# Kernel optimization log

Measured on AMD Instinct MI355X. Metric: run time of the kernel, lower is better.

## Reference

```python
import jax, jax.numpy as jnp
import numpy as np

B, T, D, H = 4, 2048, 1024, 16


def setup_inputs() -> dict:
    key = jax.random.key(0)
    ks = jax.random.split(key, 5)
    s = 0.02  # keep activations sane
    return {
        "x": jax.random.normal(ks[0], (B, T, D), jnp.float32),
        "Wq": jax.random.normal(ks[1], (D, D), jnp.float32) * s,
        "bq": jnp.zeros((D,), jnp.float32),
        "Wk": jax.random.normal(ks[2], (D, D), jnp.float32) * s,
        "bk": jnp.zeros((D,), jnp.float32),
        "Wv": jax.random.normal(ks[3], (D, D), jnp.float32) * s,
        "bv": jnp.zeros((D,), jnp.float32),
        "Wo": jax.random.normal(ks[4], (D, D), jnp.float32) * s,
        "bo": jnp.zeros((D,), jnp.float32),
    }


def _split_heads(t):  # (B,T,D) -> (B,H,T,d)
    b, s, d = t.shape
    return t.reshape(b, s, H, d // H).transpose(0, 2, 1, 3)


def reference(x, Wq, bq, Wk, bk, Wv, bv, Wo, bo):
    d_k = D // H
    q = _split_heads(x @ Wq + bq)  # (B,H,T,d)
    k = _split_heads(x @ Wk + bk)
    v = _split_heads(x @ Wv + bv)
    # scaled dot-product similarities (B,H,T,T)
    scores = jnp.einsum("bhqd,bhkd->bhqk", q, k) / jnp.sqrt(jnp.asarray(d_k, x.dtype))
    # causal mask: masked_fill(tril==0, -inf)
    causal = jnp.tril(jnp.ones((T, T), bool))
    scores = jnp.where(causal, scores, -jnp.inf)
    attn = jax.nn.softmax(scores, axis=-1)
    ctx = jnp.einsum("bhqk,bhkd->bhqd", attn, v)  # (B,H,T,d)
    ctx = ctx.transpose(0, 2, 1, 3).reshape(x.shape[0], T, D)
    return ctx @ Wo + bo
```

## Files before the change

kernel.cpp:

```cpp
#include <hip/hip_runtime.h>
#include <hip/hip_bf16.h>

typedef unsigned short u16;
typedef __attribute__((ext_vector_type(8))) short bf16x8;
typedef __attribute__((ext_vector_type(4))) short bf16x4;
typedef __attribute__((ext_vector_type(4))) float f32x4;

#define DD 1024
#define TT 2048
#define HH 16
#define BB 4
#define DK 64
#define MM 8192

#define QSCALE 0.180336880f

__device__ __forceinline__ u16 f2b(float x) {
  __hip_bfloat16 h = __float2bfloat16(x);
  return *reinterpret_cast<u16*>(&h);
}

#define GLD16(gp, lp)                                                         \
  __builtin_amdgcn_global_load_lds(                                           \
      (const __attribute__((address_space(1))) unsigned int*)(gp),            \
      (__attribute__((address_space(3))) unsigned int*)(lp), 16, 0, 0)

__global__ __launch_bounds__(256) void cast_bf16_kernel(
    const float* __restrict__ src, u16* __restrict__ dst, int n) {
  int i = (blockIdx.x * 256 + threadIdx.x) * 4;
  if (i + 3 < n) {
    float4 v = *reinterpret_cast<const float4*>(src + i);
    ushort4 o;
    o.x = f2b(v.x); o.y = f2b(v.y); o.z = f2b(v.z); o.w = f2b(v.w);
    *reinterpret_cast<ushort4*>(dst + i) = o;
  }
}

__global__ __launch_bounds__(256) void transpose_cast_kernel(
    const float* __restrict__ W0, const float* __restrict__ W1,
    const float* __restrict__ W2, const float* __restrict__ W3,
    u16* __restrict__ O0, u16* __restrict__ O1,
    u16* __restrict__ O2, u16* __restrict__ O3) {
  const float* W; u16* O;
  switch (blockIdx.z) {
    case 0: W = W0; O = O0; break;
    case 1: W = W1; O = O1; break;
    case 2: W = W2; O = O2; break;
    default: W = W3; O = O3; break;
  }
  __shared__ float tile[32][33];
  int tx = threadIdx.x, ty = threadIdx.y;
  int bx = blockIdx.x * 32;
  int by = blockIdx.y * 32;
#pragma unroll
  for (int j = 0; j < 4; j++)
    tile[ty + j * 8][tx] = W[(size_t)(by + ty + j * 8) * DD + bx + tx];
  __syncthreads();
#pragma unroll
  for (int j = 0; j < 4; j++)
    O[(size_t)(bx + ty + j * 8) * DD + by + tx] = f2b(tile[tx][ty + j * 8]);
}

__global__ __launch_bounds__(256) void gemm_qkv_kernel(
    const u16* __restrict__ A,
    const u16* __restrict__ WtQ, const u16* __restrict__ WtK,
    const u16* __restrict__ WtV,
    const float* __restrict__ bq, const float* __restrict__ bk,
    const float* __restrict__ bv,
    u16* __restrict__ Qo, u16* __restrict__ Ko, u16* __restrict__ Vo) {
  __shared__ __align__(16) u16 As[128 * 32];
  __shared__ __align__(16) u16 Bs[128 * 32];
  int z = blockIdx.z;
  const u16* Bt = (z == 0) ? WtQ : ((z == 1) ? WtK : WtV);
  const float* bias = (z == 0) ? bq : ((z == 1) ? bk : bv);
  int tid = threadIdx.x;
  int wave = tid >> 6, lane = tid & 63;
  int quad = lane >> 4, l16 = lane & 15;
  int m0 = blockIdx.x * 128, n0 = blockIdx.y * 128;
  int wm = (wave >> 1) * 64, wn = (wave & 1) * 64;

  f32x4 acc[4][4];
#pragma unroll
  for (int i = 0; i < 4; i++)
#pragma unroll
    for (int j = 0; j < 4; j++) acc[i][j] = (f32x4){0.f, 0.f, 0.f, 0.f};

  for (int k0 = 0; k0 < DD; k0 += 32) {
#pragma unroll
    for (int c = 0; c < 2; c++) {
      int idx = tid * 8 + c * 2048;
      int row = idx >> 5, kk = idx & 31;
      GLD16(A + (size_t)(m0 + row) * DD + k0 + kk, As + idx);
      GLD16(Bt + (size_t)(n0 + row) * DD + k0 + kk, Bs + idx);
    }
    __syncthreads();
    bf16x8 af[4], bfr[4];
#pragma unroll
    for (int mb = 0; mb < 4; mb++)
      af[mb] = *reinterpret_cast<const bf16x8*>(&As[(wm + mb * 16 + l16) * 32 + quad * 8]);
#pragma unroll
    for (int nb = 0; nb < 4; nb++)
      bfr[nb] = *reinterpret_cast<const bf16x8*>(&Bs[(wn + nb * 16 + l16) * 32 + quad * 8]);
    if (z != 2) {
#pragma unroll
      for (int mb = 0; mb < 4; mb++)
#pragma unroll
        for (int nb = 0; nb < 4; nb++)
          acc[mb][nb] = __builtin_amdgcn_mfma_f32_16x16x32_bf16(
              af[mb], bfr[nb], acc[mb][nb], 0, 0, 0);
    } else {
#pragma unroll
      for (int mb = 0; mb < 4; mb++)
#pragma unroll
        for (int nb = 0; nb < 4; nb++)
          acc[mb][nb] = __builtin_amdgcn_mfma_f32_16x16x32_bf16(
              bfr[nb], af[mb], acc[mb][nb], 0, 0, 0);
    }
    __syncthreads();
  }

  if (z == 2) {
    int b = m0 >> 11;
    int tbase = (m0 & 2047) + wm;
#pragma unroll
    for (int nb = 0; nb < 4; nb++)
#pragma unroll
      for (int r = 0; r < 4; r++) {
        int ncol = n0 + wn + nb * 16 + quad * 4 + r;
        int h = ncol >> 6, dd = ncol & 63;
        float bv2 = bias[ncol];
        u16* basep = Vo + (((size_t)(b * HH + h) * DK) + dd) * TT;
#pragma unroll
        for (int mb = 0; mb < 4; mb++) {
          int t = tbase + mb * 16 + l16;
          basep[t] = f2b(acc[mb][nb][r] + bv2);
        }
      }
    return;
  }

  u16* outp = (z == 0) ? Qo : Ko;
  float scale = (z == 0) ? QSCALE : 1.0f;
#pragma unroll
  for (int mb = 0; mb < 4; mb++) {
#pragma unroll
    for (int nb = 0; nb < 4; nb++) {
      int col = n0 + wn + nb * 16 + l16;
      float bv2 = bias[col];
#pragma unroll
      for (int r = 0; r < 4; r++) {
        int row = m0 + wm + mb * 16 + quad * 4 + r;
        float val = (acc[mb][nb][r] + bv2) * scale;
        int hh = col >> 6, dd = col & 63;
        int b = row >> 11, t = row & 2047;
        outp[(((size_t)(b * HH + hh) * TT) + t) * DK + dd] = f2b(val);
      }
    }
  }
}

__global__ __launch_bounds__(256) void gemm_out_kernel(
    const u16* __restrict__ A, const u16* __restrict__ Bt,
    const float* __restrict__ bias, float* __restrict__ outp) {
  __shared__ __align__(16) u16 As[128 * 32];
  __shared__ __align__(16) u16 Bs[128 * 32];
  int tid = threadIdx.x;
  int wave = tid >> 6, lane = tid & 63;
  int quad = lane >> 4, l16 = lane & 15;
  int m0 = blockIdx.x * 128, n0 = blockIdx.y * 128;
  int wm = (wave >> 1) * 64, wn = (wave & 1) * 64;

  f32x4 acc[4][4];
#pragma unroll
  for (int i = 0; i < 4; i++)
#pragma unroll
    for (int j = 0; j < 4; j++) acc[i][j] = (f32x4){0.f, 0.f, 0.f, 0.f};

  for (int k0 = 0; k0 < DD; k0 += 32) {
#pragma unroll
    for (int c = 0; c < 2; c++) {
      int idx = tid * 8 + c * 2048;
      int row = idx >> 5, kk = idx & 31;
      GLD16(A + (size_t)(m0 + row) * DD + k0 + kk, As + idx);
      GLD16(Bt + (size_t)(n0 + row) * DD + k0 + kk, Bs + idx);
    }
    __syncthreads();
    bf16x8 af[4], bfr[4];
#pragma unroll
    for (int mb = 0; mb < 4; mb++)
      af[mb] = *reinterpret_cast<const bf16x8*>(&As[(wm + mb * 16 + l16) * 32 + quad * 8]);
#pragma unroll
    for (int nb = 0; nb < 4; nb++)
      bfr[nb] = *reinterpret_cast<const bf16x8*>(&Bs[(wn + nb * 16 + l16) * 32 + quad * 8]);
#pragma unroll
    for (int mb = 0; mb < 4; mb++)
#pragma unroll
      for (int nb = 0; nb < 4; nb++)
        acc[mb][nb] = __builtin_amdgcn_mfma_f32_16x16x32_bf16(
            af[mb], bfr[nb], acc[mb][nb], 0, 0, 0);
    __syncthreads();
  }

#pragma unroll
  for (int mb = 0; mb < 4; mb++) {
#pragma unroll
    for (int nb = 0; nb < 4; nb++) {
      int col = n0 + wn + nb * 16 + l16;
      float bv = bias[col];
#pragma unroll
      for (int r = 0; r < 4; r++) {
        int row = m0 + wm + mb * 16 + quad * 4 + r;
        outp[(size_t)row * DD + col] = acc[mb][nb][r] + bv;
      }
    }
  }
}

__global__ __launch_bounds__(1024, 4) void attn_kernel(
    const u16* __restrict__ Q, const u16* __restrict__ K,
    const u16* __restrict__ VT, u16* __restrict__ ctx) {
  __shared__ __align__(16) u16 smem[4][64][72];
  __shared__ float fbuf[16][16];

  int tid = threadIdx.x;
  int wave = tid >> 6, lane = tid & 63;
  int quad = lane >> 4, l16 = lane & 15;
  int bid = blockIdx.x;
  int bh = bid & 63;
  int px = bid >> 6;
  int b = bh >> 4, h = bh & 15;
  const u16* Qh = Q + (size_t)bh * TT * DK;
  const u16* Kh = K + (size_t)bh * TT * DK;
  const u16* Vh = VT + (size_t)bh * DK * TT;
  int sidx = tid * 4;
  int srow = sidx >> 6, scol = sidx & 63;

  for (int phase = 0; phase < 2; phase++) {
    int qt = phase ? (7 - px) : px;
    int ktmax = 4 * qt + 3;
    int dtile = 4 * qt + (wave >> 2);
    int qrl = (wave * 16 + l16) & 63;
    __syncthreads();

    const u16* qrow = Qh + (size_t)(qt * 256 + wave * 16 + l16) * DK + quad * 8;
    bf16x8 qf0 = *reinterpret_cast<const bf16x8*>(qrow);
    bf16x8 qf1 = *reinterpret_cast<const bf16x8*>(qrow + 32);

    uint2 kpre = *reinterpret_cast<const uint2*>(Kh + sidx);
    uint2 vpre = *reinterpret_cast<const uint2*>(Vh + (size_t)srow * TT + scol);
    *reinterpret_cast<uint2*>(&smem[0][srow][scol]) = kpre;
    *reinterpret_cast<uint2*>(&smem[2][srow][scol]) = vpre;
    __syncthreads();

    f32x4 oacc[4];
#pragma unroll
    for (int dt = 0; dt < 4; dt++) oacc[dt] = (f32x4){0.f, 0.f, 0.f, 0.f};
    float lsum = 0.f;

    for (int kt = 0; kt <= ktmax; kt++) {
      int cur = kt & 1, nxt = cur ^ 1;
      bool more = kt < ktmax;
      if (more) {
        kpre = *reinterpret_cast<const uint2*>(Kh + (size_t)(kt + 1) * 4096 + sidx);
        vpre = *reinterpret_cast<const uint2*>(
            Vh + (size_t)srow * TT + (kt + 1) * 64 + scol);
      }

      if (kt <= dtile) {
        f32x4 sacc[4];
#pragma unroll
        for (int kb = 0; kb < 4; kb++) sacc[kb] = (f32x4){0.f, 0.f, 0.f, 0.f};
#pragma unroll
        for (int kb = 0; kb < 4; kb++) {
          bf16x8 kf0 = *reinterpret_cast<const bf16x8*>(&smem[cur][kb * 16 + l16][quad * 8]);
          bf16x8 kf1 = *reinterpret_cast<const bf16x8*>(&smem[cur][kb * 16 + l16][32 + quad * 8]);
          sacc[kb] = __builtin_amdgcn_mfma_f32_16x16x32_bf16(kf0, qf0, sacc[kb], 0, 0, 0);
          sacc[kb] = __builtin_amdgcn_mfma_f32_16x16x32_bf16(kf1, qf1, sacc[kb], 0, 0, 0);
        }

        if (kt == dtile) {
#pragma unroll
          for (int kb = 0; kb < 4; kb++)
#pragma unroll
            for (int r = 0; r < 4; r++)
              if (kb * 16 + quad * 4 + r > qrl) sacc[kb][r] = -__builtin_inff();
        }

#pragma unroll
        for (int kb = 0; kb < 4; kb++) {
          float p0 = exp2f(sacc[kb][0]), p1 = exp2f(sacc[kb][1]);
          float p2 = exp2f(sacc[kb][2]), p3 = exp2f(sacc[kb][3]);
          lsum += (p0 + p1) + (p2 + p3);
          union { unsigned u[2]; bf16x4 v; } pk;
          pk.u[0] = (unsigned)f2b(p0) | ((unsigned)f2b(p1) << 16);
          pk.u[1] = (unsigned)f2b(p2) | ((unsigned)f2b(p3) << 16);
#pragma unroll
          for (int dt = 0; dt < 4; dt++) {
            bf16x4 vf = *reinterpret_cast<const bf16x4*>(
                &smem[2 + cur][dt * 16 + l16][kb * 16 + quad * 4]);
            oacc[dt] = __builtin_amdgcn_mfma_f32_16x16x16bf16_1k(pk.v, vf, oacc[dt], 0, 0, 0);
          }
        }
      }

      if (more) {
        *reinterpret_cast<uint2*>(&smem[nxt][srow][scol]) = kpre;
        *reinterpret_cast<uint2*>(&smem[2 + nxt][srow][scol]) = vpre;
      }
      __syncthreads();
    }

    lsum += __shfl_xor(lsum, 16);
    lsum += __shfl_xor(lsum, 32);
    if (quad == 0) fbuf[wave][l16] = lsum;
    asm volatile("s_waitcnt lgkmcnt(0)" ::: "memory");
    f32x4 lv = *reinterpret_cast<const f32x4*>(&fbuf[wave][quad * 4]);
    f32x4 inv;
#pragma unroll
    for (int r = 0; r < 4; r++) inv[r] = 1.0f / lv[r];

    u16* Obuf = &smem[0][0][0];
#pragma unroll
    for (int dt = 0; dt < 4; dt++)
#pragma unroll
      for (int r = 0; r < 4; r++)
        Obuf[(wave * 16 + quad * 4 + r) * 72 + dt * 16 + l16] =
            f2b(oacc[dt][r] * inv[r]);
    asm volatile("s_waitcnt lgkmcnt(0)" ::: "memory");
#pragma unroll
    for (int i = 0; i < 2; i++) {
      int idx = lane * 8 + i * 512;
      int row = idx >> 6, colc = idx & 63;
      uint4 v = *reinterpret_cast<const uint4*>(&Obuf[(wave * 16 + row) * 72 + colc]);
      int t = qt * 256 + wave * 16 + row;
      *reinterpret_cast<uint4*>(
          ctx + ((size_t)(b * TT + t)) * DD + h * DK + colc) = v;
    }
  }
}

extern "C" void kernel_launch(void* const* d_in, const int* in_sizes, int n_in,
                              void* d_out, int out_size, void* d_ws, size_t ws_size,
                              hipStream_t stream) {
  const float* x  = (const float*)d_in[0];
  const float* Wq = (const float*)d_in[1];
  const float* bq = (const float*)d_in[2];
  const float* Wk = (const float*)d_in[3];
  const float* bk = (const float*)d_in[4];
  const float* Wv = (const float*)d_in[5];
  const float* bv = (const float*)d_in[6];
  const float* Wo = (const float*)d_in[7];
  const float* bo = (const float*)d_in[8];
  float* out = (float*)d_out;

  char* ws = (char*)d_ws;
  size_t off = 0;
  u16* xb  = (u16*)(ws + off); off += (size_t)MM * DD * 2;
  u16* wtq = (u16*)(ws + off); off += (size_t)DD * DD * 2;
  u16* wtk = (u16*)(ws + off); off += (size_t)DD * DD * 2;
  u16* wtv = (u16*)(ws + off); off += (size_t)DD * DD * 2;
  u16* wto = (u16*)(ws + off); off += (size_t)DD * DD * 2;
  u16* Qb  = (u16*)(ws + off); off += (size_t)MM * DD * 2;
  u16* Kb  = (u16*)(ws + off); off += (size_t)MM * DD * 2;
  u16* VTb = (u16*)(ws + off); off += (size_t)MM * DD * 2;
  u16* ctx = (u16*)(ws + off); off += (size_t)MM * DD * 2;

  {
    int n = MM * DD;
    cast_bf16_kernel<<<n / 1024, 256, 0, stream>>>(x, xb, n);
  }
  {
    dim3 grid(DD / 32, DD / 32, 4);
    dim3 block(32, 8);
    transpose_cast_kernel<<<grid, block, 0, stream>>>(Wq, Wk, Wv, Wo, wtq, wtk, wtv, wto);
  }
  {
    dim3 grid(MM / 128, DD / 128, 3);
    gemm_qkv_kernel<<<grid, 256, 0, stream>>>(xb, wtq, wtk, wtv, bq, bk, bv,
                                              Qb, Kb, VTb);
  }
  {
    attn_kernel<<<256, 1024, 0, stream>>>(Qb, Kb, VTb, ctx);
  }
  {
    dim3 grid(MM / 128, DD / 128);
    gemm_out_kernel<<<grid, 256, 0, stream>>>(ctx, wto, bo, out);
  }
}
```

Baseline: 275.4 us.

## Restructure attention into 4-wave blocks, each wave handling two query sub-tiles

The attention kernel now launches 512 blocks of 256 threads instead of 256 blocks of 1024 threads, with 128-query tiles. Each wave computes two 16-row query fragments (A and B) against each shared K/V tile, so every K/V fragment read from LDS is reused twice and the causal work split is reorganised. The change trades higher per-wave register pressure for more independent blocks and less LDS traffic per MFMA. The final write-back now needs a block-wide sync.

Measured after the change: 388.5 us. +41.1%, slower.

```diff
diff --git a/kernel.cpp b/kernel.cpp
--- a/kernel.cpp
+++ b/kernel.cpp
@@ -216,11 +216,12 @@
   }
 }
 
-__global__ __launch_bounds__(1024, 4) void attn_kernel(
+__global__ __launch_bounds__(256, 4) void attn_kernel(
     const u16* __restrict__ Q, const u16* __restrict__ K,
     const u16* __restrict__ VT, u16* __restrict__ ctx) {
-  __shared__ __align__(16) u16 smem[4][64][72];
-  __shared__ float fbuf[16][16];
+  __shared__ __align__(16) u16 Ksm[2][64][72];
+  __shared__ __align__(16) u16 Vsm[2][64][72];
+  __shared__ float fbufA[4][16], fbufB[4][16];
 
   int tid = threadIdx.x;
   int wave = tid >> 6, lane = tid & 63;
@@ -232,107 +233,168 @@
   const u16* Qh = Q + (size_t)bh * TT * DK;
   const u16* Kh = K + (size_t)bh * TT * DK;
   const u16* Vh = VT + (size_t)bh * DK * TT;
-  int sidx = tid * 4;
-  int srow = sidx >> 6, scol = sidx & 63;
 
   for (int phase = 0; phase < 2; phase++) {
-    int qt = phase ? (7 - px) : px;
-    int ktmax = 4 * qt + 3;
-    int dtile = 4 * qt + (wave >> 2);
-    int qrl = (wave * 16 + l16) & 63;
-    __syncthreads();
-
-    const u16* qrow = Qh + (size_t)(qt * 256 + wave * 16 + l16) * DK + quad * 8;
-    bf16x8 qf0 = *reinterpret_cast<const bf16x8*>(qrow);
-    bf16x8 qf1 = *reinterpret_cast<const bf16x8*>(qrow + 32);
-
-    uint2 kpre = *reinterpret_cast<const uint2*>(Kh + sidx);
-    uint2 vpre = *reinterpret_cast<const uint2*>(Vh + (size_t)srow * TT + scol);
-    *reinterpret_cast<uint2*>(&smem[0][srow][scol]) = kpre;
-    *reinterpret_cast<uint2*>(&smem[2][srow][scol]) = vpre;
-    __syncthreads();
-
-    f32x4 oacc[4];
-#pragma unroll
-    for (int dt = 0; dt < 4; dt++) oacc[dt] = (f32x4){0.f, 0.f, 0.f, 0.f};
-    float lsum = 0.f;
+    int qt = phase ? (15 - px) : px;
+    int ktmax = 2 * qt + 1;
+    int qrl = wave * 16 + l16;
+    __syncthreads();
+
+    const u16* qrowA = Qh + (size_t)(qt * 128 + wave * 16 + l16) * DK + quad * 8;
+    bf16x8 qa0 = *reinterpret_cast<const bf16x8*>(qrowA);
+    bf16x8 qa1 = *reinterpret_cast<const bf16x8*>(qrowA + 32);
+    const u16* qrowB = qrowA + (size_t)64 * DK;
+    bf16x8 qb0 = *reinterpret_cast<const bf16x8*>(qrowB);
+    bf16x8 qb1 = *reinterpret_cast<const bf16x8*>(qrowB + 32);
+
+    uint4 kpre[2], vpre[2];
+#pragma unroll
+    for (int c = 0; c < 2; c++) {
+      int idx = tid * 8 + c * 2048;
+      kpre[c] = *reinterpret_cast<const uint4*>(Kh + idx);
+      vpre[c] = *reinterpret_cast<const uint4*>(Vh + (size_t)(idx >> 6) * TT + (idx & 63));
+    }
+#pragma unroll
+    for (int c = 0; c < 2; c++) {
+      int idx = tid * 8 + c * 2048;
+      *reinterpret_cast<uint4*>(&Ksm[0][idx >> 6][idx & 63]) = kpre[c];
+      *reinterpret_cast<uint4*>(&Vsm[0][idx >> 6][idx & 63]) = vpre[c];
+    }
+    __syncthreads();
+
+    f32x4 oaccA[4], oaccB[4];
+#pragma unroll
+    for (int dt = 0; dt < 4; dt++) {
+      oaccA[dt] = (f32x4){0.f, 0.f, 0.f, 0.f};
+      oaccB[dt] = (f32x4){0.f, 0.f, 0.f, 0.f};
+    }
+    float lsA = 0.f, lsB = 0.f;
 
     for (int kt = 0; kt <= ktmax; kt++) {
       int cur = kt & 1, nxt = cur ^ 1;
       bool more = kt < ktmax;
+      bool doA = kt <= 2 * qt;
       if (more) {
-        kpre = *reinterpret_cast<const uint2*>(Kh + (size_t)(kt + 1) * 4096 + sidx);
-        vpre = *reinterpret_cast<const uint2*>(
-            Vh + (size_t)srow * TT + (kt + 1) * 64 + scol);
-      }
-
-      if (kt <= dtile) {
-        f32x4 sacc[4];
-#pragma unroll
-        for (int kb = 0; kb < 4; kb++) sacc[kb] = (f32x4){0.f, 0.f, 0.f, 0.f};
-#pragma unroll
-        for (int kb = 0; kb < 4; kb++) {
-          bf16x8 kf0 = *reinterpret_cast<const bf16x8*>(&smem[cur][kb * 16 + l16][quad * 8]);
-          bf16x8 kf1 = *reinterpret_cast<const bf16x8*>(&smem[cur][kb * 16 + l16][32 + quad * 8]);
-          sacc[kb] = __builtin_amdgcn_mfma_f32_16x16x32_bf16(kf0, qf0, sacc[kb], 0, 0, 0);
-          sacc[kb] = __builtin_amdgcn_mfma_f32_16x16x32_bf16(kf1, qf1, sacc[kb], 0, 0, 0);
-        }
-
-        if (kt == dtile) {
-#pragma unroll
-          for (int kb = 0; kb < 4; kb++)
-#pragma unroll
-            for (int r = 0; r < 4; r++)
-              if (kb * 16 + quad * 4 + r > qrl) sacc[kb][r] = -__builtin_inff();
-        }
-
-#pragma unroll
-        for (int kb = 0; kb < 4; kb++) {
-          float p0 = exp2f(sacc[kb][0]), p1 = exp2f(sacc[kb][1]);
-          float p2 = exp2f(sacc[kb][2]), p3 = exp2f(sacc[kb][3]);
-          lsum += (p0 + p1) + (p2 + p3);
+#pragma unroll
+        for (int c = 0; c < 2; c++) {
+          int idx = tid * 8 + c * 2048;
+          kpre[c] = *reinterpret_cast<const uint4*>(Kh + (size_t)(kt + 1) * 4096 + idx);
+          vpre[c] = *reinterpret_cast<const uint4*>(
+              Vh + (size_t)(idx >> 6) * TT + (kt + 1) * 64 + (idx & 63));
+        }
+      }
+
+      f32x4 sA[4], sB[4];
+#pragma unroll
+      for (int kb = 0; kb < 4; kb++) {
+        sA[kb] = (f32x4){0.f, 0.f, 0.f, 0.f};
+        sB[kb] = (f32x4){0.f, 0.f, 0.f, 0.f};
+      }
+#pragma unroll
+      for (int kb = 0; kb < 4; kb++) {
+        bf16x8 kf0 = *reinterpret_cast<const bf16x8*>(&Ksm[cur][kb * 16 + l16][quad * 8]);
+        bf16x8 kf1 = *reinterpret_cast<const bf16x8*>(&Ksm[cur][kb * 16 + l16][32 + quad * 8]);
+        if (doA) {
+          sA[kb] = __builtin_amdgcn_mfma_f32_16x16x32_bf16(kf0, qa0, sA[kb], 0, 0, 0);
+          sA[kb] = __builtin_amdgcn_mfma_f32_16x16x32_bf16(kf1, qa1, sA[kb], 0, 0, 0);
+        }
+        sB[kb] = __builtin_amdgcn_mfma_f32_16x16x32_bf16(kf0, qb0, sB[kb], 0, 0, 0);
+        sB[kb] = __builtin_amdgcn_mfma_f32_16x16x32_bf16(kf1, qb1, sB[kb], 0, 0, 0);
+      }
+
+      if (kt == 2 * qt) {
+#pragma unroll
+        for (int kb = 0; kb < 4; kb++)
+#pragma unroll
+          for (int r = 0; r < 4; r++)
+            if (kb * 16 + quad * 4 + r > qrl) sA[kb][r] = -__builtin_inff();
+      }
+      if (kt == ktmax) {
+#pragma unroll
+        for (int kb = 0; kb < 4; kb++)
+#pragma unroll
+          for (int r = 0; r < 4; r++)
+            if (kb * 16 + quad * 4 + r > qrl) sB[kb][r] = -__builtin_inff();
+      }
+
+      bf16x4 pkA[4], pkB[4];
+#pragma unroll
+      for (int kb = 0; kb < 4; kb++) {
+        if (doA) {
+          float p0 = exp2f(sA[kb][0]), p1 = exp2f(sA[kb][1]);
+          float p2 = exp2f(sA[kb][2]), p3 = exp2f(sA[kb][3]);
+          lsA += (p0 + p1) + (p2 + p3);
           union { unsigned u[2]; bf16x4 v; } pk;
           pk.u[0] = (unsigned)f2b(p0) | ((unsigned)f2b(p1) << 16);
           pk.u[1] = (unsigned)f2b(p2) | ((unsigned)f2b(p3) << 16);
-#pragma unroll
-          for (int dt = 0; dt < 4; dt++) {
-            bf16x4 vf = *reinterpret_cast<const bf16x4*>(
-                &smem[2 + cur][dt * 16 + l16][kb * 16 + quad * 4]);
-            oacc[dt] = __builtin_amdgcn_mfma_f32_16x16x16bf16_1k(pk.v, vf, oacc[dt], 0, 0, 0);
-          }
-        }
-      }
+          pkA[kb] = pk.v;
+        }
+        float q0 = exp2f(sB[kb][0]), q1 = exp2f(sB[kb][1]);
+        float q2 = exp2f(sB[kb][2]), q3 = exp2f(sB[kb][3]);
+        lsB += (q0 + q1) + (q2 + q3);
+        union { unsigned u[2]; bf16x4 v; } pk2;
+        pk2.u[0] = (unsigned)f2b(q0) | ((unsigned)f2b(q1) << 16);
+        pk2.u[1] = (unsigned)f2b(q2) | ((unsigned)f2b(q3) << 16);
+        pkB[kb] = pk2.v;
+      }
+
+#pragma unroll
+      for (int kb = 0; kb < 4; kb++)
+#pragma unroll
+        for (int dt = 0; dt < 4; dt++) {
+          bf16x4 vf = *reinterpret_cast<const bf16x4*>(
+              &Vsm[cur][dt * 16 + l16][kb * 16 + quad * 4]);
+          if (doA)
+            oaccA[dt] = __builtin_amdgcn_mfma_f32_16x16x16bf16_1k(pkA[kb], vf, oaccA[dt], 0, 0, 0);
+          oaccB[dt] = __builtin_amdgcn_mfma_f32_16x16x16bf16_1k(pkB[kb], vf, oaccB[dt], 0, 0, 0);
+        }
 
       if (more) {
-        *reinterpret_cast<uint2*>(&smem[nxt][srow][scol]) = kpre;
-        *reinterpret_cast<uint2*>(&smem[2 + nxt][srow][scol]) = vpre;
+#pragma unroll
+        for (int c = 0; c < 2; c++) {
+          int idx = tid * 8 + c * 2048;
+          *reinterpret_cast<uint4*>(&Ksm[nxt][idx >> 6][idx & 63]) = kpre[c];
+          *reinterpret_cast<uint4*>(&Vsm[nxt][idx >> 6][idx & 63]) = vpre[c];
+        }
       }
       __syncthreads();
     }
 
-    lsum += __shfl_xor(lsum, 16);
-    lsum += __shfl_xor(lsum, 32);
-    if (quad == 0) fbuf[wave][l16] = lsum;
+    lsA += __shfl_xor(lsA, 16);
+    lsA += __shfl_xor(lsA, 32);
+    lsB += __shfl_xor(lsB, 16);
+    lsB += __shfl_xor(lsB, 32);
+    if (quad == 0) {
+      fbufA[wave][l16] = lsA;
+      fbufB[wave][l16] = lsB;
+    }
     asm volatile("s_waitcnt lgkmcnt(0)" ::: "memory");
-    f32x4 lv = *reinterpret_cast<const f32x4*>(&fbuf[wave][quad * 4]);
-    f32x4 inv;
-#pragma unroll
-    for (int r = 0; r < 4; r++) inv[r] = 1.0f / lv[r];
-
-    u16* Obuf = &smem[0][0][0];
+    f32x4 lvA = *reinterpret_cast<const f32x4*>(&fbufA[wave][quad * 4]);
+    f32x4 lvB = *reinterpret_cast<const f32x4*>(&fbufB[wave][quad * 4]);
+    f32x4 invA, invB;
+#pragma unroll
+    for (int r = 0; r < 4; r++) {
+      invA[r] = 1.0f / lvA[r];
+      invB[r] = 1.0f / lvB[r];
+    }
+
+    u16* Obuf = &Ksm[0][0][0];
 #pragma unroll
     for (int dt = 0; dt < 4; dt++)
 #pragma unroll
-      for (int r = 0; r < 4; r++)
+      for (int r = 0; r < 4; r++) {
         Obuf[(wave * 16 + quad * 4 + r) * 72 + dt * 16 + l16] =
-            f2b(oacc[dt][r] * inv[r]);
-    asm volatile("s_waitcnt lgkmcnt(0)" ::: "memory");
-#pragma unroll
-    for (int i = 0; i < 2; i++) {
-      int idx = lane * 8 + i * 512;
+            f2b(oaccA[dt][r] * invA[r]);
+        Obuf[(64 + wave * 16 + quad * 4 + r) * 72 + dt * 16 + l16] =
+            f2b(oaccB[dt][r] * invB[r]);
+      }
+    __syncthreads();
+#pragma unroll
+    for (int i = 0; i < 4; i++) {
+      int idx = tid * 8 + i * 2048;
       int row = idx >> 6, colc = idx & 63;
-      uint4 v = *reinterpret_cast<const uint4*>(&Obuf[(wave * 16 + row) * 72 + colc]);
-      int t = qt * 256 + wave * 16 + row;
+      uint4 v = *reinterpret_cast<const uint4*>(&Obuf[row * 72 + colc]);
+      int t = qt * 128 + row;
       *reinterpret_cast<uint4*>(
           ctx + ((size_t)(b * TT + t)) * DD + h * DK + colc) = v;
     }
@@ -380,7 +442,7 @@
                                               Qb, Kb, VTb);
   }
   {
-    attn_kernel<<<256, 1024, 0, stream>>>(Qb, Kb, VTb, ctx);
+    attn_kernel<<<512, 256, 0, stream>>>(Qb, Kb, VTb, ctx);
   }
   {
     dim3 grid(MM / 128, DD / 128);
```
